# Performance work log

Hardware: AMD Instinct MI355X
Metric: run time of the kernel (lower is better)

The kernel has to match this reference:

```python
import jax, jax.numpy as jnp
import numpy as np

PATCH = 16  # conv kernel size == stride


def _patch_embed(im, W, b):
    # im: (B, C, H, W) NCHW; W: (hidden, C, s, s); returns (B, h, w, hidden)
    out = jax.lax.conv_general_dilated(
        im, W, window_strides=(PATCH, PATCH), padding='VALID',
        dimension_numbers=('NCHW', 'OIHW', 'NCHW'))
    out = out + b[None, :, None, None]
    return jnp.transpose(out, (0, 2, 3, 1))  # (B, h, w, hidden)


def setup_inputs() -> dict:
    key = jax.random.key(0)
    k1, k2, k3, k4 = jax.random.split(key, 4)
    B, C, H, Wd = 64, 3, 224, 224
    hidden = 384
    x = jax.random.normal(k1, (B, C, H, Wd), dtype=jnp.float32)
    y = jax.random.normal(k2, (B, C, H, Wd), dtype=jnp.float32)
    fan_in = C * PATCH * PATCH
    bound = 1.0 / np.sqrt(fan_in)
    W = jax.random.uniform(k3, (hidden, C, PATCH, PATCH), dtype=jnp.float32,
                           minval=-bound, maxval=bound)
    b = jax.random.uniform(k4, (hidden,), dtype=jnp.float32,
                           minval=-bound, maxval=bound)
    return {'x': x, 'y': y, 'W': W, 'b': b}


def reference(x, y, W, b):
    B = x.shape[0]
    xp = _patch_embed(x, W, b)  # (B, h, w, C)
    yp = _patch_embed(y, W, b)  # (B, h, w, C)
    h, w = xp.shape[1], xp.shape[2]
    logp = jax.nn.log_softmax(xp, axis=-1)          # (B, h, w, C)
    q = jax.lax.stop_gradient(jax.nn.softmax(yp, axis=-1))  # detached targets
    # CE[i, j] = mean over (h, w) of -(q_j * logp_i).sum(-1)
    # Faithful factorization of the (B, B, h, w, C) broadcast in the original.
    CE = -jnp.einsum('ihwc,jhwc->ij', logp, q) / (h * w)  # (B, B)
    close = jnp.trace(CE) / B
    far = (CE.sum() - jnp.trace(CE)) / (B * B - B)
    return close / far
```

## Files before the change

kernel.cpp:

```cpp
#include <hip/hip_runtime.h>

#define HID   384
#define K_PE  768
#define IMGST 150528
#define NCOLS 75264

typedef unsigned short ushort_t;
using f32x4  = __attribute__((ext_vector_type(4))) float;
using short8 = __attribute__((ext_vector_type(8))) short;

__device__ __forceinline__ unsigned bfpack(float lo, float hi) {
    union { float f; unsigned u; } a, b; a.f = lo; b.f = hi;
    unsigned ra = (a.u + 0x7fffu + ((a.u >> 16) & 1u)) >> 16;
    unsigned rb = (b.u + 0x7fffu + ((b.u >> 16) & 1u)) & 0xffff0000u;
    return ra | rb;
}

__global__ __launch_bounds__(256) void prep(const float* __restrict__ W,
                                            ushort_t* __restrict__ Wfrag,
                                            float* __restrict__ scal,
                                            float* __restrict__ Lsum,
                                            float* __restrict__ Qsum) {
    const int t = blockIdx.x * 256 + threadIdx.x;
    if (t < 4) scal[t] = 0.f;
    if (t < NCOLS / 4) {
        ((float4*)Lsum)[t] = float4{0.f, 0.f, 0.f, 0.f};
        ((float4*)Qsum)[t] = float4{0.f, 0.f, 0.f, 0.f};
    }
    if (t < 36864) {
        const int n  = t / 96;
        const int ko = t % 96;
        const float4 a = *(const float4*)(W + (size_t)n * K_PE + ko * 8);
        const float4 b = *(const float4*)(W + (size_t)n * K_PE + ko * 8 + 4);
        uint4 p;
        p.x = bfpack(a.x, a.y); p.y = bfpack(a.z, a.w);
        p.z = bfpack(b.x, b.y); p.w = bfpack(b.z, b.w);
        const int nt   = n >> 4;
        const int kc   = ko >> 2;
        const int lane = (ko & 3) * 16 + (n & 15);
        ((uint4*)Wfrag)[(nt * 24 + kc) * 64 + lane] = p;
    }
}

__global__ __launch_bounds__(256, 4) void pe_all(
    const float* __restrict__ xin, const float* __restrict__ yin,
    const ushort_t* __restrict__ Wfrag, const float* __restrict__ bias,
    float* __restrict__ scal, float* __restrict__ Lsum,
    float* __restrict__ Qsum) {
    const int p  = blockIdx.x;
    const int ig = blockIdx.y;
    const int pi = p / 14;
    const int pj = p - pi * 14;

    __shared__ __align__(16) ushort_t As[2][2][16 * 64];
    __shared__ float Smx[4][16], Ssx[4][16], Smy[4][16], Ssy[4][16];
    __shared__ float sT[4];

    const int tid  = threadIdx.x;
    const int wave = tid >> 6;
    const int lane = tid & 63;
    const int lm   = lane & 15;
    const int lq   = lane >> 4;
    const int wn   = wave * 96;

    const int z  = tid >> 7;
    const int sm = (tid >> 3) & 15;
    const int qt = tid & 7;
    const float* ab = (z ? yin : xin) +
                      (size_t)(ig * 16 + sm) * IMGST + pi * 3584 + pj * 16;
    ushort_t* awp = &As[z][0][sm * 64 + ((qt ^ (sm & 7)) * 8)];

    int ard[2];
#pragma unroll
    for (int ks = 0; ks < 2; ++ks)
        ard[ks] = lm * 64 + (((ks * 4 + lq) ^ (lm & 7)) * 8);

    const ushort_t* bbase = Wfrag + (size_t)lane * 8;

    f32x4 accx[6] = {};
    f32x4 accy[6] = {};

#define STAGE(KB, BUF)                                                       \
    {                                                                        \
        const int k0  = (KB) + qt * 8;                                       \
        const int off = (k0 >> 8) * 50176 + (((k0 >> 4) & 15) * 224) + (k0 & 15); \
        float4 f0 = *(const float4*)(ab + off);                              \
        float4 f1 = *(const float4*)(ab + off + 4);                          \
        uint4 px;                                                            \
        px.x = bfpack(f0.x, f0.y); px.y = bfpack(f0.z, f0.w);                \
        px.z = bfpack(f1.x, f1.y); px.w = bfpack(f1.z, f1.w);                \
        *(uint4*)(awp + (BUF) * 1024) = px;                                  \
    }

    STAGE(0, 0)
    __syncthreads();

    for (int kbi = 0; kbi < 12; ++kbi) {
        const int cur = kbi & 1;
        if (kbi < 11) STAGE(kbi * 64 + 64, cur ^ 1)
#pragma unroll
        for (int ks = 0; ks < 2; ++ks) {
            short8 bfr[6];
#pragma unroll
            for (int ni = 0; ni < 6; ++ni)
                bfr[ni] = *(const short8*)(bbase +
                          (size_t)(((wave * 6 + ni) * 24 + kbi * 2 + ks) * 64) * 8);
            short8 afx = *(const short8*)&As[0][cur][ard[ks]];
            short8 afy = *(const short8*)&As[1][cur][ard[ks]];
#pragma unroll
            for (int ni = 0; ni < 6; ++ni) {
                accx[ni] = __builtin_amdgcn_mfma_f32_16x16x32_bf16(
                    afx, bfr[ni], accx[ni], 0, 0, 0);
                accy[ni] = __builtin_amdgcn_mfma_f32_16x16x32_bf16(
                    afy, bfr[ni], accy[ni], 0, 0, 0);
            }
        }
        __syncthreads();
    }
#undef STAGE

#pragma unroll
    for (int ni = 0; ni < 6; ++ni) {
        const float bv = bias[wn + ni * 16 + lm];
#pragma unroll
        for (int r = 0; r < 4; ++r) {
            accx[ni][r] += bv;
            accy[ni][r] += bv;
        }
    }

    float mx[4], my_[4];
#pragma unroll
    for (int r = 0; r < 4; ++r) {
        float a = accx[0][r], b = accy[0][r];
#pragma unroll
        for (int ni = 1; ni < 6; ++ni) {
            a = fmaxf(a, accx[ni][r]);
            b = fmaxf(b, accy[ni][r]);
        }
        mx[r] = a; my_[r] = b;
    }
#pragma unroll
    for (int off = 1; off < 16; off <<= 1)
#pragma unroll
        for (int r = 0; r < 4; ++r) {
            mx[r]  = fmaxf(mx[r],  __shfl_xor(mx[r],  off));
            my_[r] = fmaxf(my_[r], __shfl_xor(my_[r], off));
        }
    if (lm == 0)
#pragma unroll
        for (int r = 0; r < 4; ++r) {
            Smx[wave][lq * 4 + r] = mx[r];
            Smy[wave][lq * 4 + r] = my_[r];
        }
    __syncthreads();
#pragma unroll
    for (int r = 0; r < 4; ++r) {
        const int row = lq * 4 + r;
        mx[r]  = fmaxf(fmaxf(Smx[0][row], Smx[1][row]),
                       fmaxf(Smx[2][row], Smx[3][row]));
        my_[r] = fmaxf(fmaxf(Smy[0][row], Smy[1][row]),
                       fmaxf(Smy[2][row], Smy[3][row]));
    }

    float sx[4], sy[4];
#pragma unroll
    for (int r = 0; r < 4; ++r) {
        float a = 0.f, b = 0.f;
#pragma unroll
        for (int ni = 0; ni < 6; ++ni) {
            a += __expf(accx[ni][r] - mx[r]);
            b += __expf(accy[ni][r] - my_[r]);
        }
        sx[r] = a; sy[r] = b;
    }
#pragma unroll
    for (int off = 1; off < 16; off <<= 1)
#pragma unroll
        for (int r = 0; r < 4; ++r) {
            sx[r] += __shfl_xor(sx[r], off);
            sy[r] += __shfl_xor(sy[r], off);
        }
    if (lm == 0)
#pragma unroll
        for (int r = 0; r < 4; ++r) {
            Ssx[wave][lq * 4 + r] = sx[r];
            Ssy[wave][lq * 4 + r] = sy[r];
        }
    __syncthreads();
#pragma unroll
    for (int r = 0; r < 4; ++r) {
        const int row = lq * 4 + r;
        const float ssx = Ssx[0][row] + Ssx[1][row] + Ssx[2][row] + Ssx[3][row];
        const float ssy = Ssy[0][row] + Ssy[1][row] + Ssy[2][row] + Ssy[3][row];
        sx[r] = mx[r] + __logf(ssx);
        sy[r] = 1.f / ssy;
    }

    float T = 0.f;
    float cL[6], cQ[6];
#pragma unroll
    for (int ni = 0; ni < 6; ++ni) { cL[ni] = 0.f; cQ[ni] = 0.f; }
#pragma unroll
    for (int r = 0; r < 4; ++r) {
        const float sh  = sx[r];
        const float m   = my_[r];
        const float inv = sy[r];
#pragma unroll
        for (int ni = 0; ni < 6; ++ni) {
            const float lp = accx[ni][r] - sh;
            const float qv = __expf(accy[ni][r] - m) * inv;
            T += lp * qv;
            cL[ni] += lp;
            cQ[ni] += qv;
        }
    }
#pragma unroll
    for (int ni = 0; ni < 6; ++ni) {
        cL[ni] += __shfl_xor(cL[ni], 16); cL[ni] += __shfl_xor(cL[ni], 32);
        cQ[ni] += __shfl_xor(cQ[ni], 16); cQ[ni] += __shfl_xor(cQ[ni], 32);
    }
    if (lq == 0)
#pragma unroll
        for (int ni = 0; ni < 6; ++ni) {
            const int col = p * HID + wn + ni * 16 + lm;
            atomicAdd(&Lsum[col], cL[ni]);
            atomicAdd(&Qsum[col], cQ[ni]);
        }
#pragma unroll
    for (int off = 32; off > 0; off >>= 1) T += __shfl_xor(T, off);
    if (lane == 0) sT[wave] = T;
    __syncthreads();
    if (tid == 0)
        atomicAdd(&scal[0], sT[0] + sT[1] + sT[2] + sT[3]);
}

__global__ __launch_bounds__(256) void final_dot(const float* __restrict__ Lsum,
                                                 const float* __restrict__ Qsum,
                                                 float* __restrict__ scal,
                                                 float* __restrict__ out) {
    const int idx = blockIdx.x * 256 + threadIdx.x;
    float s = 0.f;
    if (idx < NCOLS / 4) {
        float4 a = ((const float4*)Lsum)[idx];
        float4 b = ((const float4*)Qsum)[idx];
        s = a.x * b.x + a.y * b.y + a.z * b.z + a.w * b.w;
    }
#pragma unroll
    for (int off = 32; off > 0; off >>= 1) s += __shfl_xor(s, off);
    __shared__ float sS[4];
    __shared__ int lastflag;
    if ((threadIdx.x & 63) == 0) sS[threadIdx.x >> 6] = s;
    __syncthreads();
    if (threadIdx.x == 0) {
        atomicAdd(&scal[1], sS[0] + sS[1] + sS[2] + sS[3]);
        __threadfence();
        int old = atomicAdd((int*)&scal[3], 1);
        lastflag = (old == (int)gridDim.x - 1);
    }
    __syncthreads();
    if (lastflag && threadIdx.x == 0) {
        float S = atomicAdd(&scal[1], 0.f);
        float T = atomicAdd(&scal[0], 0.f);
        out[0] = 63.f * T / (S - T);
    }
}

extern "C" void kernel_launch(void* const* d_in, const int* in_sizes, int n_in,
                              void* d_out, int out_size, void* d_ws, size_t ws_size,
                              hipStream_t stream) {
    const float* x = (const float*)d_in[0];
    const float* y = (const float*)d_in[1];
    const float* W = (const float*)d_in[2];
    const float* b = (const float*)d_in[3];
    float* out = (float*)d_out;

    float*    scal  = (float*)d_ws;
    float*    Lsum  = scal + 16;
    float*    Qsum  = Lsum + NCOLS;
    ushort_t* Wfrag = (ushort_t*)(Qsum + NCOLS);

    prep<<<148, 256, 0, stream>>>(W, Wfrag, scal, Lsum, Qsum);
    pe_all<<<dim3(196, 4), 256, 0, stream>>>(x, y, Wfrag, b, scal, Lsum, Qsum);
    final_dot<<<74, 256, 0, stream>>>(Lsum, Qsum, scal, out);
}
```

Baseline: 154.6 us.

## Stage full patch K-slab into LDS once and drop per-iteration barriers

Instead of double-buffering 64-wide K slices of the image patches and syncing every iteration, each block now loads all 768 K values for its 16 images of x and y into LDS up front, converting to bf16. The MFMA loop is then fully unrolled with no barriers inside. This raises LDS use to about 48KB per block, so the occupancy hint drops from 4 to 3 blocks. The tradeoff is that global loads no longer overlap with compute within a block, leaving latency hiding to other resident blocks.

```diff
diff --git a/kernel.cpp b/kernel.cpp
--- a/kernel.cpp
+++ b/kernel.cpp
@@ -42,7 +42,7 @@
     }
 }
 
-__global__ __launch_bounds__(256, 4) void pe_all(
+__global__ __launch_bounds__(256, 3) void pe_all(
     const float* __restrict__ xin, const float* __restrict__ yin,
     const ushort_t* __restrict__ Wfrag, const float* __restrict__ bias,
     float* __restrict__ scal, float* __restrict__ Lsum,
@@ -52,7 +52,7 @@
     const int pi = p / 14;
     const int pj = p - pi * 14;
 
-    __shared__ __align__(16) ushort_t As[2][2][16 * 64];
+    __shared__ __align__(16) ushort_t As[2][16 * 768];
     __shared__ float Smx[4][16], Ssx[4][16], Smy[4][16], Ssy[4][16];
     __shared__ float sT[4];
 
@@ -63,41 +63,41 @@
     const int lq   = lane >> 4;
     const int wn   = wave * 96;
 
-    const int z  = tid >> 7;
-    const int sm = (tid >> 3) & 15;
-    const int qt = tid & 7;
-    const float* ab = (z ? yin : xin) +
-                      (size_t)(ig * 16 + sm) * IMGST + pi * 3584 + pj * 16;
-    ushort_t* awp = &As[z][0][sm * 64 + ((qt ^ (sm & 7)) * 8)];
-
-    int ard[2];
-#pragma unroll
-    for (int ks = 0; ks < 2; ++ks)
-        ard[ks] = lm * 64 + (((ks * 4 + lq) ^ (lm & 7)) * 8);
+    {
+        const int z    = tid >> 7;
+        const int tt   = tid & 127;
+        const int simg = tt >> 3;
+        const int qt   = tt & 7;
+        const float* ab = (z ? yin : xin) +
+                          (size_t)(ig * 16 + simg) * IMGST + pi * 3584 + pj * 16;
+        ushort_t* lb = &As[z][simg * 768];
+#pragma unroll
+        for (int j = 0; j < 6; ++j) {
+            const int rr = qt + j * 8;
+            const float* ap = ab + (rr >> 4) * 50176 + (rr & 15) * 224;
+            float4 f0 = *(const float4*)(ap);
+            float4 f1 = *(const float4*)(ap + 4);
+            float4 f2 = *(const float4*)(ap + 8);
+            float4 f3 = *(const float4*)(ap + 12);
+            uint4 p0, p1;
+            p0.x = bfpack(f0.x, f0.y); p0.y = bfpack(f0.z, f0.w);
+            p0.z = bfpack(f1.x, f1.y); p0.w = bfpack(f1.z, f1.w);
+            p1.x = bfpack(f2.x, f2.y); p1.y = bfpack(f2.z, f2.w);
+            p1.z = bfpack(f3.x, f3.y); p1.w = bfpack(f3.z, f3.w);
+            const int c0 = rr * 2;
+            *(uint4*)&lb[((c0    ) ^ (simg & 7)) * 8] = p0;
+            *(uint4*)&lb[((c0 + 1) ^ (simg & 7)) * 8] = p1;
+        }
+    }
 
     const ushort_t* bbase = Wfrag + (size_t)lane * 8;
-
     f32x4 accx[6] = {};
     f32x4 accy[6] = {};
 
-#define STAGE(KB, BUF)                                                       \
-    {                                                                        \
-        const int k0  = (KB) + qt * 8;                                       \
-        const int off = (k0 >> 8) * 50176 + (((k0 >> 4) & 15) * 224) + (k0 & 15); \
-        float4 f0 = *(const float4*)(ab + off);                              \
-        float4 f1 = *(const float4*)(ab + off + 4);                          \
-        uint4 px;                                                            \
-        px.x = bfpack(f0.x, f0.y); px.y = bfpack(f0.z, f0.w);                \
-        px.z = bfpack(f1.x, f1.y); px.w = bfpack(f1.z, f1.w);                \
-        *(uint4*)(awp + (BUF) * 1024) = px;                                  \
-    }
-
-    STAGE(0, 0)
-    __syncthreads();
-
+    __syncthreads();
+
+#pragma unroll
     for (int kbi = 0; kbi < 12; ++kbi) {
-        const int cur = kbi & 1;
-        if (kbi < 11) STAGE(kbi * 64 + 64, cur ^ 1)
 #pragma unroll
         for (int ks = 0; ks < 2; ++ks) {
             short8 bfr[6];
@@ -105,8 +105,10 @@
             for (int ni = 0; ni < 6; ++ni)
                 bfr[ni] = *(const short8*)(bbase +
                           (size_t)(((wave * 6 + ni) * 24 + kbi * 2 + ks) * 64) * 8);
-            short8 afx = *(const short8*)&As[0][cur][ard[ks]];
-            short8 afy = *(const short8*)&As[1][cur][ard[ks]];
+            const int aoff = lm * 768 +
+                             (kbi * 8 + ((ks * 4 + lq) ^ (lm & 7))) * 8;
+            short8 afx = *(const short8*)&As[0][aoff];
+            short8 afy = *(const short8*)&As[1][aoff];
 #pragma unroll
             for (int ni = 0; ni < 6; ++ni) {
                 accx[ni] = __builtin_amdgcn_mfma_f32_16x16x32_bf16(
@@ -115,9 +117,7 @@
                     afy, bfr[ni], accy[ni], 0, 0, 0);
             }
         }
-        __syncthreads();
-    }
-#undef STAGE
+    }
 
 #pragma unroll
     for (int ni = 0; ni < 6; ++ni) {
```

Result: slower. 164.4 us (+6.4%).
